# Optimization experiments

Measured on AMD Instinct MI355X. Metric: run time of the kernel, lower is better.

The kernel has to match this reference:

```python
import jax, jax.numpy as jnp
import numpy as np

B, S, D, H, DH = 2, 4096, 768, 12, 64
L = 2                      # encoder layers (reduced-depth longformer-base)
HW = 256                   # one-sided sliding window (attention_window = 512)
C = 2 * HW                 # query chunk size
NC = S // C                # number of chunks
KW = C + 2 * HW            # key-window length per chunk
V = 50265
SEP_ID, NSEP = 2, 32       # </s> token id; SEPs per block (fixed by construction)
G = NSEP + 1               # global tokens: <s> at pos 0 + all SEPs
NCLS = 5
EPS = 1e-5
NEG = -1e9


def layer_norm(x, gb):
    m = jnp.mean(x, -1, keepdims=True)
    v = jnp.var(x, -1, keepdims=True)
    return (x - m) * jax.lax.rsqrt(v + EPS) * gb[0] + gb[1]


def split_heads(x):  # [B,S,D] -> [B,H,S,DH]
    return x.reshape(B, S, H, DH).transpose(0, 2, 1, 3)


def window_gather(x):  # [B,H,S,DH] -> [B,H,NC,KW,DH] overlapping key windows
    xp = jnp.pad(x, ((0, 0), (0, 0), (HW, HW), (0, 0)))
    idx = (jnp.arange(NC) * C)[:, None] + jnp.arange(KW)[None, :]
    return xp[:, :, idx, :]


def longformer_attn(x, amask, gpos, wqkv, bqkv, wqkv_g, bqkv_g, wo, bo):
    q = split_heads(x @ wqkv[0] + bqkv[0]) / np.float32(np.sqrt(DH))
    k = split_heads(x @ wqkv[1] + bqkv[1])
    v = split_heads(x @ wqkv[2] + bqkv[2])

    # ----- local sliding-window scores (banded, chunked) -----
    kw = window_gather(k)
    vw = window_gather(v)
    qc = q.reshape(B, H, NC, C, DH)
    s_loc = jnp.einsum('bhncd,bhnkd->bhnck', qc, kw)  # [B,H,NC,C,KW]

    rel = jnp.arange(KW)[None, :] - jnp.arange(C)[:, None]          # [C,KW]
    band_ok = (rel >= 0) & (rel <= 2 * HW)
    key_pos = (jnp.arange(NC) * C)[:, None] + jnp.arange(KW)[None, :] - HW
    in_b = (key_pos >= 0) & (key_pos < S)                            # [NC,KW]
    amp = jnp.pad(amask, ((0, 0), (HW, HW)))
    idx = (jnp.arange(NC) * C)[:, None] + jnp.arange(KW)[None, :]
    am_w = amp[:, idx] > 0                                           # [B,NC,KW]
    mask = band_ok[None, None, None] & in_b[None, None, :, None, :] & am_w[:, None, :, None, :]
    s_loc = jnp.where(mask, s_loc, NEG).reshape(B, H, S, KW)

    # ----- scores of every query against the G global keys -----
    gidx = gpos[:, None, :, None]                                    # [B,1,G,1]
    kg = jnp.take_along_axis(k, gidx, axis=2)                        # [B,H,G,DH]
    vg = jnp.take_along_axis(v, gidx, axis=2)
    s_glob = jnp.einsum('bhsd,bhgd->bhsg', q, kg)                    # [B,H,S,G]

    probs = jax.nn.softmax(jnp.concatenate([s_glob, s_loc], -1), -1)
    pg, pl = probs[..., :G], probs[..., G:]
    ctx = jnp.einsum('bhsg,bhgd->bhsd', pg, vg)
    ctx = ctx + jnp.einsum('bhnck,bhnkd->bhncd', pl.reshape(B, H, NC, C, KW), vw).reshape(B, H, S, DH)

    # ----- global tokens attend to everything (separate projections) -----
    qg = split_heads(x @ wqkv_g[0] + bqkv_g[0]) / np.float32(np.sqrt(DH))
    kgf = split_heads(x @ wqkv_g[1] + bqkv_g[1])
    vgf = split_heads(x @ wqkv_g[2] + bqkv_g[2])
    qg = jnp.take_along_axis(qg, gidx, axis=2)                       # [B,H,G,DH]
    s_g = jnp.einsum('bhgd,bhsd->bhgs', qg, kgf)                     # [B,H,G,S]
    s_g = jnp.where(amask[:, None, None, :] > 0, s_g, NEG)
    og = jnp.einsum('bhgs,bhsd->bhgd', jax.nn.softmax(s_g, -1), vgf)

    ctx_m = ctx.transpose(0, 2, 1, 3).reshape(B, S, D)
    og_m = og.transpose(0, 2, 1, 3).reshape(B, G, D)
    ctx_m = ctx_m.at[jnp.arange(B)[:, None], gpos].set(og_m)         # replace global rows
    return ctx_m @ wo + bo


def setup_inputs() -> dict:
    key = jax.random.key(0)
    ks = jax.random.split(key, 12)
    ids = jax.random.randint(ks[0], (B, S), 5, V, dtype=jnp.int32)
    sep_positions = (jnp.arange(NSEP) + 1) * (S // NSEP) - 1         # SEP every 128 toks
    ids = ids.at[:, sep_positions].set(SEP_ID).at[:, 0].set(0)       # <s> at pos 0
    att = jnp.ones((B, S), jnp.int32)

    def nrm(k, shp):
        return jax.random.normal(k, shp, jnp.float32) * 0.02

    ln = jnp.stack([jnp.ones(D, jnp.float32), jnp.zeros(D, jnp.float32)])
    return dict(
        input_ids=ids, attention_mask=att,
        word_emb=nrm(ks[1], (V, D)), pos_emb=nrm(ks[2], (S + 2, D)),
        type_emb=nrm(ks[3], (D,)), emb_ln=ln,
        Wqkv=nrm(ks[4], (L, 3, D, D)), bqkv=jnp.zeros((L, 3, D), jnp.float32),
        Wqkv_g=nrm(ks[5], (L, 3, D, D)), bqkv_g=jnp.zeros((L, 3, D), jnp.float32),
        Wo=nrm(ks[6], (L, D, D)), bo=jnp.zeros((L, D), jnp.float32),
        ln1=jnp.broadcast_to(ln, (L, 2, D)),
        Wff1=nrm(ks[7], (L, D, 4 * D)), bff1=jnp.zeros((L, 4 * D), jnp.float32),
        Wff2=nrm(ks[8], (L, 4 * D, D)), bff2=jnp.zeros((L, D), jnp.float32),
        ln2=jnp.broadcast_to(ln, (L, 2, D)),
        cls_W=nrm(ks[9], (NCLS, D)), cls_b=jnp.zeros((NCLS,), jnp.float32),
    )


def reference(input_ids, attention_mask, word_emb, pos_emb, type_emb, emb_ln,
              Wqkv, bqkv, Wqkv_g, bqkv_g, Wo, bo, ln1, Wff1, bff1, Wff2, bff2,
              ln2, cls_W, cls_b):
    # global attention mask: pos 0 + every SEP (fixed count by construction)
    sep_pos = jnp.sort(jnp.where(input_ids == SEP_ID, jnp.arange(S)[None, :], S), -1)[:, :NSEP]
    sep_pos = sep_pos.astype(jnp.int32)
    gpos = jnp.concatenate([jnp.zeros((B, 1), jnp.int32), sep_pos], 1)  # [B,G]

    x = word_emb[input_ids] + pos_emb[jnp.arange(S) + 2][None] + type_emb
    x = layer_norm(x, emb_ln)
    for l in range(L):
        a = longformer_attn(x, attention_mask, gpos, Wqkv[l], bqkv[l],
                            Wqkv_g[l], bqkv_g[l], Wo[l], bo[l])
        x = layer_norm(x + a, ln1[l])
        f = jax.nn.gelu(x @ Wff1[l] + bff1[l], approximate=False) @ Wff2[l] + bff2[l]
        x = layer_norm(x + f, ln2[l])

    # gather SEP embeddings (row-major over batch then sentence) -> classifier
    h = jnp.take_along_axis(x, sep_pos[:, :, None], axis=1).reshape(B * NSEP, D)
    return h @ cls_W.T + cls_b
```

## Files before the change

kernel.cpp:

```cpp
#include <hip/hip_runtime.h>


#define Bb 2
#define Ss 4096
#define Dd 768
#define Hh 12
#define Gg 33
#define NSEPn 32
#define Ll 2
#define SPAD 4640
#define PADL 256
#define NCLSn 5
#define NCH 16
#define PARTF 1056
#define PSTR 72

typedef unsigned short u16;
typedef __attribute__((ext_vector_type(8))) short bv8;
typedef __attribute__((ext_vector_type(4))) short sv4;
typedef __attribute__((ext_vector_type(4))) float f32x4;

__device__ __forceinline__ float bf2f(u16 u) {
  unsigned v = ((unsigned)u) << 16;
  return __builtin_bit_cast(float, v);
}
__device__ __forceinline__ u16 f2bf(float f) {
  unsigned u = __builtin_bit_cast(unsigned, f);
  u += 0x7fffu + ((u >> 16) & 1u);
  return (u16)(u >> 16);
}
__device__ __forceinline__ void glds16(const void* g, void* l) {
  __builtin_amdgcn_global_load_lds(
      (const __attribute__((address_space(1))) void*)g,
      (__attribute__((address_space(3))) void*)l, 16, 0, 0);
}

__global__ void sep_find_kernel(const int* __restrict__ ids, int* __restrict__ cnt,
                                int* __restrict__ list) {
  int i = blockIdx.x * 256 + threadIdx.x;
  if (i >= Bb * Ss) return;
  int b = i >> 12;
  if (ids[i] == 2) {
    int idx = atomicAdd(&cnt[b], 1);
    if (idx < 64) list[b * 64 + idx] = i & (Ss - 1);
  }
}

__global__ void sep_sort_kernel(const int* __restrict__ cnt, const int* __restrict__ list,
                                int* __restrict__ gpos) {
  int b = blockIdx.x;
  int t = threadIdx.x;
  int n = cnt[b]; if (n > 64) n = 64;
  if (t < Gg) gpos[b * Gg + t] = (t == 0) ? 0 : (Ss - 1);
  __syncthreads();
  if (t < n) {
    int v = list[b * 64 + t];
    int rank = 0;
    for (int j = 0; j < n; ++j) rank += (list[b * 64 + j] < v) ? 1 : 0;
    if (rank < NSEPn) gpos[b * Gg + 1 + rank] = v;
  }
}

__global__ __launch_bounds__(256)
void wconv_kernel(const float* __restrict__ src0, u16* __restrict__ dst0,
                  int K, int N, int grp, int sstr, long unit, long WLs) {
  __shared__ float t[32][33];
  int z = blockIdx.z;
  const float* src = src0 + (size_t)((z / grp) * sstr + (z % grp)) * K * N;
  u16* dst = dst0 + (size_t)(z / grp) * WLs + (size_t)(z % grp) * unit;
  int n0 = blockIdx.x * 32, k0 = blockIdx.y * 32;
  int tx = threadIdx.x & 31, ty = threadIdx.x >> 5;
  #pragma unroll
  for (int i = 0; i < 4; ++i)
    t[ty + i * 8][tx] = src[(size_t)(k0 + ty + i * 8) * N + n0 + tx];
  __syncthreads();
  #pragma unroll
  for (int i = 0; i < 4; ++i)
    dst[(size_t)(n0 + ty + i * 8) * K + k0 + tx] = f2bf(t[tx][ty + i * 8]);
}

__global__ __launch_bounds__(256)
void embed_ln_kernel(const int* __restrict__ ids, const float* __restrict__ we,
                     const float* __restrict__ pe, const float* __restrict__ te,
                     const float* __restrict__ lnp, float* __restrict__ x,
                     u16* __restrict__ xb) {
  int row = blockIdx.x;
  int s = row & (Ss - 1);
  int id = ids[row];
  int tid = threadIdx.x;
  float v[3]; float sm = 0.f, s2 = 0.f;
  #pragma unroll
  for (int i = 0; i < 3; ++i) {
    int c = tid + i * 256;
    float t = we[(size_t)id * Dd + c] + pe[(size_t)(s + 2) * Dd + c] + te[c];
    v[i] = t; sm += t; s2 += t * t;
  }
  __shared__ float r1[256], r2[256];
  r1[tid] = sm; r2[tid] = s2; __syncthreads();
  for (int o = 128; o; o >>= 1) {
    if (tid < o) { r1[tid] += r1[tid + o]; r2[tid] += r2[tid + o]; }
    __syncthreads();
  }
  float mean = r1[0] * (1.f / 768.f);
  float var  = r2[0] * (1.f / 768.f) - mean * mean;
  float rs = rsqrtf(var + 1e-5f);
  #pragma unroll
  for (int i = 0; i < 3; ++i) {
    int c = tid + i * 256;
    float o = (v[i] - mean) * rs * lnp[c] + lnp[Dd + c];
    x[(size_t)row * Dd + c] = o;
    xb[(size_t)row * Dd + c] = f2bf(o);
  }
}

__global__ __launch_bounds__(256)
void add_ln3_kernel(const float* __restrict__ xin, const float* __restrict__ y0,
                    const float* __restrict__ y1, const float* __restrict__ lnp,
                    float* __restrict__ xout, u16* __restrict__ xbout) {
  int row = blockIdx.x;
  int tid = threadIdx.x;
  float v[3]; float sm = 0.f, s2 = 0.f;
  #pragma unroll
  for (int i = 0; i < 3; ++i) {
    int c = tid + i * 256;
    size_t idx = (size_t)row * Dd + c;
    float t = xin[idx] + y0[idx] + y1[idx];
    v[i] = t; sm += t; s2 += t * t;
  }
  __shared__ float r1[256], r2[256];
  r1[tid] = sm; r2[tid] = s2; __syncthreads();
  for (int o = 128; o; o >>= 1) {
    if (tid < o) { r1[tid] += r1[tid + o]; r2[tid] += r2[tid + o]; }
    __syncthreads();
  }
  float mean = r1[0] * (1.f / 768.f);
  float var  = r2[0] * (1.f / 768.f) - mean * mean;
  float rs = rsqrtf(var + 1e-5f);
  #pragma unroll
  for (int i = 0; i < 3; ++i) {
    int c = tid + i * 256;
    float o = (v[i] - mean) * rs * lnp[c] + lnp[Dd + c];
    xout[(size_t)row * Dd + c] = o;
    xbout[(size_t)row * Dd + c] = f2bf(o);
  }
}

template <int MODE>
__global__ __launch_bounds__(256)
void gemm2_kernel(const u16* __restrict__ A, const u16* __restrict__ Bt,
                  const float* __restrict__ bias, float* __restrict__ outf,
                  float* __restrict__ outf2,
                  u16* __restrict__ o0, u16* __restrict__ o1, u16* __restrict__ o2,
                  u16* __restrict__ o3, u16* __restrict__ o4,
                  int N, int Ks, int Kl, float scale) {
  __shared__ u16 la[2][128 * 32], lb[2][128 * 32];
  int tid = threadIdx.x;
  int wave = tid >> 6, lane = tid & 63;
  int wr = wave >> 1, wc = wave & 1;
  int lg = lane >> 4, lc = lane & 15;
  int row0 = blockIdx.y * 128, col0 = blockIdx.x * 128;
  int koff = blockIdx.z * Kl;

  const u16* Ag = A + (size_t)(row0 + wave * 32 + (lane >> 2)) * Ks + (lane & 3) * 8 + koff;
  const u16* Bg = Bt + (size_t)(col0 + wave * 32 + (lane >> 2)) * Ks + (lane & 3) * 8 + koff;
  int wofs = wave * 1024;

  f32x4 acc[4][4];
  #pragma unroll
  for (int m = 0; m < 4; ++m)
    #pragma unroll
    for (int n = 0; n < 4; ++n) acc[m][n] = (f32x4){0.f, 0.f, 0.f, 0.f};

  glds16(Ag, la[0] + wofs);
  glds16(Ag + (size_t)16 * Ks, la[0] + wofs + 512);
  glds16(Bg, lb[0] + wofs);
  glds16(Bg + (size_t)16 * Ks, lb[0] + wofs + 512);
  __syncthreads();

  int nk = Kl >> 5;
  for (int t = 0; t < nk; ++t) {
    int cur = t & 1;
    if (t + 1 < nk) {
      int k1 = (t + 1) << 5;
      glds16(Ag + k1, la[cur ^ 1] + wofs);
      glds16(Ag + (size_t)16 * Ks + k1, la[cur ^ 1] + wofs + 512);
      glds16(Bg + k1, lb[cur ^ 1] + wofs);
      glds16(Bg + (size_t)16 * Ks + k1, lb[cur ^ 1] + wofs + 512);
    }
    bv8 af[4], bf_[4];
    #pragma unroll
    for (int m = 0; m < 4; ++m)
      af[m] = *reinterpret_cast<const bv8*>(la[cur] + (wr * 64 + m * 16 + lc) * 32 + lg * 8);
    #pragma unroll
    for (int n = 0; n < 4; ++n)
      bf_[n] = *reinterpret_cast<const bv8*>(lb[cur] + (wc * 64 + n * 16 + lc) * 32 + lg * 8);
    __builtin_amdgcn_s_setprio(1);
    #pragma unroll
    for (int m = 0; m < 4; ++m)
      #pragma unroll
      for (int n = 0; n < 4; ++n)
        acc[m][n] = __builtin_amdgcn_mfma_f32_16x16x32_bf16(af[m], bf_[n], acc[m][n], 0, 0, 0);
    __builtin_amdgcn_s_setprio(0);
    __syncthreads();
  }

  #pragma unroll
  for (int m = 0; m < 4; ++m) {
    int grow0 = row0 + wr * 64 + m * 16 + lg * 4;
    #pragma unroll
    for (int n = 0; n < 4; ++n) {
      int gcol = col0 + wc * 64 + n * 16 + lc;
      float bvl = bias[gcol];
      if (MODE == 0) {
        float* od = blockIdx.z ? outf2 : outf;
        float badd = blockIdx.z ? 0.f : bvl;
        #pragma unroll
        for (int r = 0; r < 4; ++r)
          od[(size_t)(grow0 + r) * N + gcol] = acc[m][n][r] + badd;
      } else if (MODE == 1) {
        #pragma unroll
        for (int r = 0; r < 4; ++r) {
          float v = acc[m][n][r] + bvl;
          v = 0.5f * v * (1.0f + erff(v * 0.70710678118654752f));
          o0[(size_t)(grow0 + r) * N + gcol] = f2bf(v);
        }
      } else if (MODE == 4) {
        #pragma unroll
        for (int r = 0; r < 4; ++r)
          o0[(size_t)(grow0 + r) * N + gcol] = f2bf((acc[m][n][r] + bvl) * scale);
      } else if (MODE == 2) {
        int sec = (col0 >> 7) / 6;
        int colr = gcol - sec * 768;
        int hh = colr >> 6, d = colr & 63;
        int bb = grow0 >> 12, s = grow0 & (Ss - 1);
        size_t bhh = (size_t)(bb * Hh + hh);
        if (sec == 0) {
          #pragma unroll
          for (int r = 0; r < 4; ++r)
            o0[(bhh * Ss + s + r) * 64 + d] = f2bf((acc[m][n][r] + bvl) * scale);
        } else if (sec == 1) {
          #pragma unroll
          for (int r = 0; r < 4; ++r)
            o1[(bhh * SPAD + PADL + s + r) * 64 + d] = f2bf(acc[m][n][r] + bvl);
        } else if (sec == 2) {
          sv4 pk;
          #pragma unroll
          for (int r = 0; r < 4; ++r) pk[r] = (short)f2bf(acc[m][n][r] + bvl);
          *reinterpret_cast<sv4*>(o2 + (bhh * 64 + d) * SPAD + PADL + s) = pk;
        } else if (sec == 3) {
          #pragma unroll
          for (int r = 0; r < 4; ++r)
            o3[(bhh * Ss + s + r) * 64 + d] = f2bf(acc[m][n][r] + bvl);
        } else {
          sv4 pk;
          #pragma unroll
          for (int r = 0; r < 4; ++r) pk[r] = (short)f2bf(acc[m][n][r] + bvl);
          *reinterpret_cast<sv4*>(o4 + (bhh * 64 + d) * Ss + s) = pk;
        }
      }
    }
  }
}

__global__ __launch_bounds__(256)
void gather_glob_kernel(const u16* __restrict__ kpk, const u16* __restrict__ vtpk,
                        const int* __restrict__ gpos, u16* __restrict__ kg,
                        u16* __restrict__ vgt) {
  int bh = blockIdx.x;
  int b = bh / Hh;
  int tid = threadIdx.x;
  for (int idx = tid; idx < 64 * 64; idx += 256) {
    int g = idx >> 6, d = idx & 63;
    u16 kv = 0, vv = 0;
    if (g < Gg) {
      int p = gpos[b * Gg + g];
      kv = kpk[((size_t)bh * SPAD + PADL + p) * 64 + d];
      vv = vtpk[((size_t)bh * 64 + d) * SPAD + PADL + p];
    }
    kg[(size_t)bh * 4096 + idx] = kv;
    vgt[((size_t)bh * 64 + d) * 64 + g] = vv;
  }
}

__global__ __launch_bounds__(256)
void gather_xg_kernel(const u16* __restrict__ xb, const int* __restrict__ gpos,
                      u16* __restrict__ xg) {
  int rg = blockIdx.x;
  int b = rg / Gg;
  int p = gpos[rg];
  int tid = threadIdx.x;
  for (int c = tid; c < Dd; c += 256)
    xg[(size_t)rg * Dd + c] = xb[((size_t)b * Ss + p) * Dd + c];
}

#define LOCAL_NB (Bb * Hh * (Ss / 64))
__global__ __launch_bounds__(256)
void attn_local_kernel(const u16* __restrict__ qpk, const u16* __restrict__ kpk,
                       const u16* __restrict__ vtpk, const u16* __restrict__ kg,
                       const u16* __restrict__ vgt, const int* __restrict__ amask,
                       u16* __restrict__ ctx) {
  __shared__ u16 Plds[4][16 * PSTR];
  int bid = blockIdx.x;
  int swz = (bid & 7) * (LOCAL_NB / 8) + (bid >> 3);
  int qb = swz & 63;
  int bh = swz >> 6;
  int b = bh / Hh;
  int h = bh - b * Hh;
  int wv = threadIdx.x >> 6;
  int q0 = qb * 64 + wv * 16;
  int lane = threadIdx.x & 63;
  int lg = lane >> 4, lc = lane & 15;
  int lg4 = lg * 4;
  int q = q0 + lc;

  const u16* qbase = qpk + (((size_t)bh) * Ss + q0) * 64;
  bv8 aq0 = *reinterpret_cast<const bv8*>(qbase + (size_t)lc * 64 + lg * 8);
  bv8 aq1 = *reinterpret_cast<const bv8*>(qbase + (size_t)lc * 64 + 32 + lg * 8);

  f32x4 o[4];
  #pragma unroll
  for (int i = 0; i < 4; ++i) o[i] = (f32x4){0.f, 0.f, 0.f, 0.f};
  float mrun = -1e30f, lrun = 0.f;

  const u16* kgb = kg + ((size_t)bh) * 64 * 64;
  const u16* vgb = vgt + ((size_t)bh) * 64 * 64;
  const u16* kb = kpk + ((size_t)bh) * SPAD * 64;
  const u16* vb = vtpk + ((size_t)bh) * 64 * SPAD;
  const int* amb = amask + b * Ss;
  u16* P = &Plds[wv][0];

  bv8 kc[8];
  #pragma unroll
  for (int j = 0; j < 4; ++j) {
    const u16* kr = kgb + (size_t)(j * 16 + lc) * 64;
    kc[2 * j]     = *reinterpret_cast<const bv8*>(kr + lg * 8);
    kc[2 * j + 1] = *reinterpret_cast<const bv8*>(kr + 32 + lg * 8);
  }
  int amvN;
  { int ni = min(max(q0 - 256 + lane, 0), Ss - 1); amvN = amb[ni]; }

  for (int step = 0; step < 10; ++step) {
    bool isg = (step == 0);
    int ks = isg ? 0 : (q0 - 256 + (step - 1) * 64);
    int amvC = amvN;
    if (step < 9) { int ni = min(max(q0 - 256 + step * 64 + lane, 0), Ss - 1); amvN = amb[ni]; }

    bv8 vf[8];
    #pragma unroll
    for (int j2 = 0; j2 < 2; ++j2)
      #pragma unroll
      for (int nt = 0; nt < 4; ++nt) {
        const u16* vr = isg ? (vgb + (size_t)(nt * 16 + lc) * 64 + j2 * 32)
                            : (vb + (size_t)(nt * 16 + lc) * SPAD + PADL + ks + j2 * 32);
        vf[j2 * 4 + nt] = *reinterpret_cast<const bv8*>(vr + lg * 8);
      }
    unsigned long long kmask;
    if (isg) {
      kmask = (1ull << Gg) - 1;
    } else {
      int kidx = ks + lane;
      kmask = __ballot((kidx >= 0) && (kidx < Ss) && (amvC > 0));
    }
    f32x4 sc[4];
    __builtin_amdgcn_s_setprio(1);
    #pragma unroll
    for (int j = 0; j < 4; ++j) {
      f32x4 z = (f32x4){0.f, 0.f, 0.f, 0.f};
      sc[j] = __builtin_amdgcn_mfma_f32_16x16x32_bf16(kc[2 * j], aq0, z, 0, 0, 0);
      sc[j] = __builtin_amdgcn_mfma_f32_16x16x32_bf16(kc[2 * j + 1], aq1, sc[j], 0, 0, 0);
    }
    __builtin_amdgcn_s_setprio(0);
    if (step < 9) {
      int ksn = q0 - 256 + step * 64;
      #pragma unroll
      for (int j = 0; j < 4; ++j) {
        const u16* kr = kb + (size_t)(PADL + ksn + j * 16 + lc) * 64;
        kc[2 * j]     = *reinterpret_cast<const bv8*>(kr + lg * 8);
        kc[2 * j + 1] = *reinterpret_cast<const bv8*>(kr + 32 + lg * 8);
      }
    }
    float mloc = -1e30f;
    bool fast = (!isg) && (step >= 2) && (step <= 8) && (kmask == ~0ull);
    if (fast) {
      #pragma unroll
      for (int j = 0; j < 4; ++j)
        #pragma unroll
        for (int r = 0; r < 4; ++r) mloc = fmaxf(mloc, sc[j][r]);
    } else {
      #pragma unroll
      for (int j = 0; j < 4; ++j)
        #pragma unroll
        for (int r = 0; r < 4; ++r) {
          int kk = ks + j * 16 + lg4 + r;
          bool ok = (kmask >> (j * 16 + lg4 + r)) & 1;
          if (!isg) ok = ok && ((unsigned)(kk - q + 256) <= 512u);
          sc[j][r] = ok ? sc[j][r] : -1e9f;
          mloc = fmaxf(mloc, sc[j][r]);
        }
    }
    mloc = fmaxf(mloc, __shfl_xor(mloc, 16));
    mloc = fmaxf(mloc, __shfl_xor(mloc, 32));
    if (__any(mloc > mrun)) {
      float nm = fmaxf(mrun, mloc);
      float scal = __expf(mrun - nm);
      mrun = nm;
      lrun *= scal;
      #pragma unroll
      for (int r = 0; r < 4; ++r) {
        float sr = __shfl(scal, lg4 + r);
        #pragma unroll
        for (int nt = 0; nt < 4; ++nt) o[nt][r] *= sr;
      }
    }
    float psum = 0.f;
    #pragma unroll
    for (int j = 0; j < 4; ++j) {
      sv4 pk;
      #pragma unroll
      for (int r = 0; r < 4; ++r) {
        float p = __expf(sc[j][r] - mrun);
        psum += p;
        pk[r] = (short)f2bf(p);
      }
      *reinterpret_cast<sv4*>(P + lc * PSTR + j * 16 + lg4) = pk;
    }
    psum += __shfl_xor(psum, 16);
    psum += __shfl_xor(psum, 32);
    lrun += psum;
    __builtin_amdgcn_s_setprio(1);
    #pragma unroll
    for (int j2 = 0; j2 < 2; ++j2) {
      bv8 ap = *reinterpret_cast<const bv8*>(P + lc * PSTR + j2 * 32 + lg * 8);
      #pragma unroll
      for (int nt = 0; nt < 4; ++nt)
        o[nt] = __builtin_amdgcn_mfma_f32_16x16x32_bf16(ap, vf[j2 * 4 + nt], o[nt], 0, 0, 0);
    }
    __builtin_amdgcn_s_setprio(0);
  }
  float inv = 1.0f / lrun;
  #pragma unroll
  for (int r = 0; r < 4; ++r) {
    float invr = __shfl(inv, lg4 + r);
    size_t rowoff = ((size_t)b * Ss + q0 + lg4 + r) * Dd + h * 64;
    #pragma unroll
    for (int nt = 0; nt < 4; ++nt)
      ctx[rowoff + nt * 16 + lc] = f2bf(o[nt][r] * invr);
  }
}

__global__ __launch_bounds__(192)
void attn_globalq_kernel(const u16* __restrict__ qgb, const u16* __restrict__ kgf,
                         const u16* __restrict__ vgt, const int* __restrict__ amask,
                         float* __restrict__ part) {
  __shared__ u16 Plds[3][16 * 32];
  int blk = blockIdx.x;
  int ch = blk & (NCH - 1);
  int bh = blk / NCH;
  int b = bh / Hh, h = bh - b * Hh;
  int wv = threadIdx.x >> 6;
  int lane = threadIdx.x & 63;
  int lg = lane >> 4, lc = lane & 15;

  int qrow = wv * 16 + lc;
  bv8 aq0 = (bv8)0, aq1 = (bv8)0;
  if (qrow < Gg) {
    const u16* qr = qgb + (size_t)(b * Gg + qrow) * Dd + h * 64;
    aq0 = *reinterpret_cast<const bv8*>(qr + lg * 8);
    aq1 = *reinterpret_cast<const bv8*>(qr + 32 + lg * 8);
  }

  f32x4 o[4];
  float mrun[4], lrun[4];
  #pragma unroll
  for (int i = 0; i < 4; ++i) { o[i] = (f32x4){0.f,0.f,0.f,0.f}; mrun[i] = -1e30f; lrun[i] = 0.f; }

  const u16* kb = kgf + ((size_t)bh) * Ss * 64;
  const u16* vb = vgt + ((size_t)bh) * 64 * Ss;
  const int* amb = amask + b * Ss;
  int ks0 = ch * (Ss / NCH);

  for (int st = 0; st < (Ss / NCH) / 32; ++st) {
    int ks = ks0 + st * 32;
    f32x4 sc0, sc1;
    {
      const u16* kr0 = kb + (size_t)(ks + lc) * 64;
      const u16* kr1 = kr0 + 16 * 64;
      bv8 b00 = *reinterpret_cast<const bv8*>(kr0 + lg * 8);
      bv8 b01 = *reinterpret_cast<const bv8*>(kr0 + 32 + lg * 8);
      bv8 b10 = *reinterpret_cast<const bv8*>(kr1 + lg * 8);
      bv8 b11 = *reinterpret_cast<const bv8*>(kr1 + 32 + lg * 8);
      f32x4 z = (f32x4){0.f,0.f,0.f,0.f};
      sc0 = __builtin_amdgcn_mfma_f32_16x16x32_bf16(aq0, b00, z, 0, 0, 0);
      sc0 = __builtin_amdgcn_mfma_f32_16x16x32_bf16(aq1, b01, sc0, 0, 0, 0);
      sc1 = __builtin_amdgcn_mfma_f32_16x16x32_bf16(aq0, b10, z, 0, 0, 0);
      sc1 = __builtin_amdgcn_mfma_f32_16x16x32_bf16(aq1, b11, sc1, 0, 0, 0);
    }
    bool v0 = amb[ks + lc] > 0;
    bool v1 = amb[ks + 16 + lc] > 0;
    #pragma unroll
    for (int r = 0; r < 4; ++r) {
      float s0 = v0 ? sc0[r] : -1e9f;
      float s1 = v1 ? sc1[r] : -1e9f;
      float rm = fmaxf(s0, s1);
      #pragma unroll
      for (int off = 1; off < 16; off <<= 1) rm = fmaxf(rm, __shfl_xor(rm, off));
      float nm = fmaxf(mrun[r], rm);
      float scal = __expf(mrun[r] - nm);
      float p0 = __expf(s0 - nm);
      float p1 = __expf(s1 - nm);
      float ps = p0 + p1;
      #pragma unroll
      for (int off = 1; off < 16; off <<= 1) ps += __shfl_xor(ps, off);
      lrun[r] = lrun[r] * scal + ps;
      mrun[r] = nm;
      #pragma unroll
      for (int nt = 0; nt < 4; ++nt) o[nt][r] *= scal;
      int prow = lg * 4 + r;
      Plds[wv][prow * 32 + lc] = f2bf(p0);
      Plds[wv][prow * 32 + 16 + lc] = f2bf(p1);
    }
    bv8 ap = *reinterpret_cast<const bv8*>(&Plds[wv][lc * 32 + lg * 8]);
    #pragma unroll
    for (int nt = 0; nt < 4; ++nt) {
      const u16* vr = vb + (size_t)(nt * 16 + lc) * Ss + ks;
      bv8 bvv = *reinterpret_cast<const bv8*>(vr + lg * 8);
      o[nt] = __builtin_amdgcn_mfma_f32_16x16x32_bf16(ap, bvv, o[nt], 0, 0, 0);
    }
  }

  float* pb = part + ((size_t)(bh * 3 + wv) * NCH + ch) * PARTF;
  #pragma unroll
  for (int r = 0; r < 4; ++r) {
    int row = lg * 4 + r;
    #pragma unroll
    for (int nt = 0; nt < 4; ++nt)
      pb[row * 64 + nt * 16 + lc] = o[nt][r];
    if (lc == 0) {
      pb[1024 + row] = mrun[r];
      pb[1040 + row] = lrun[r];
    }
  }
}

__global__ __launch_bounds__(256)
void attn_gmerge_kernel(const float* __restrict__ part, const int* __restrict__ gpos,
                        u16* __restrict__ ctx) {
  __shared__ float wgt[Gg][NCH];
  __shared__ float sinvl[Gg];
  int bh = blockIdx.x;
  int b = bh / Hh, h = bh - b * Hh;
  int tid = threadIdx.x;
  if (tid < Gg) {
    int qt = tid >> 4, rr = tid & 15;
    const float* pb = part + ((size_t)(bh * 3 + qt) * NCH) * PARTF;
    float mx = -1e30f;
    for (int c = 0; c < NCH; ++c) mx = fmaxf(mx, pb[c * PARTF + 1024 + rr]);
    float l = 0.f;
    for (int c = 0; c < NCH; ++c) {
      float w = __expf(pb[c * PARTF + 1024 + rr] - mx);
      wgt[tid][c] = w;
      l += w * pb[c * PARTF + 1040 + rr];
    }
    sinvl[tid] = 1.0f / l;
  }
  __syncthreads();
  for (int e = tid; e < Gg * 64; e += 256) {
    int row = e >> 6, d = e & 63;
    int qt = row >> 4, rr = row & 15;
    const float* pb = part + ((size_t)(bh * 3 + qt) * NCH) * PARTF + rr * 64 + d;
    float acc = 0.f;
    #pragma unroll
    for (int c = 0; c < NCH; ++c) acc += wgt[row][c] * pb[c * PARTF];
    int pos = gpos[b * Gg + row];
    ctx[((size_t)b * Ss + pos) * Dd + h * 64 + d] = f2bf(acc * sinvl[row]);
  }
}

__global__ __launch_bounds__(64)
void cls_kernel(const float* __restrict__ x, const float* __restrict__ W,
                const float* __restrict__ bias, const int* __restrict__ gpos,
                float* __restrict__ out) {
  int r = blockIdx.x;
  int b = r >> 5, i = r & 31;
  int pos = gpos[b * Gg + 1 + i];
  int lane = threadIdx.x;
  const float* xr = x + ((size_t)b * Ss + pos) * Dd;
  float acc[NCLSn] = {0.f, 0.f, 0.f, 0.f, 0.f};
  for (int k = lane; k < Dd; k += 64) {
    float xv = xr[k];
    #pragma unroll
    for (int c = 0; c < NCLSn; ++c) acc[c] += xv * W[c * Dd + k];
  }
  #pragma unroll
  for (int c = 0; c < NCLSn; ++c) {
    #pragma unroll
    for (int off = 1; off < 64; off <<= 1) acc[c] += __shfl_xor(acc[c], off);
  }
  if (lane == 0) {
    #pragma unroll
    for (int c = 0; c < NCLSn; ++c) out[r * NCLSn + c] = acc[c] + bias[c];
  }
}

extern "C" void kernel_launch(void* const* d_in, const int* in_sizes, int n_in,
                              void* d_out, int out_size, void* d_ws, size_t ws_size,
                              hipStream_t stream) {
  const int* ids     = (const int*)d_in[0];
  const int* amask   = (const int*)d_in[1];
  const float* we    = (const float*)d_in[2];
  const float* pe    = (const float*)d_in[3];
  const float* te    = (const float*)d_in[4];
  const float* embln = (const float*)d_in[5];
  const float* Wqkv  = (const float*)d_in[6];
  const float* bqkv  = (const float*)d_in[7];
  const float* Wqkvg = (const float*)d_in[8];
  const float* bqkvg = (const float*)d_in[9];
  const float* Wo    = (const float*)d_in[10];
  const float* bo    = (const float*)d_in[11];
  const float* ln1   = (const float*)d_in[12];
  const float* Wff1  = (const float*)d_in[13];
  const float* bff1  = (const float*)d_in[14];
  const float* Wff2  = (const float*)d_in[15];
  const float* bff2  = (const float*)d_in[16];
  const float* ln2   = (const float*)d_in[17];
  const float* clsW  = (const float*)d_in[18];
  const float* clsb  = (const float*)d_in[19];
  float* out = (float*)d_out;

  char* ws = (char*)d_ws;
  size_t off = 0;
  auto alloc = [&](size_t bytes) { size_t o = off; off += (bytes + 255) & ~(size_t)255; return o; };

  const size_t DD = (size_t)Dd * Dd;
  const size_t DF = (size_t)Dd * 4 * Dd;
  const size_t WL = 7 * DD + 2 * DF;

  size_t o_cnt  = alloc(Bb * 4);
  size_t o_list = alloc(Bb * 64 * 4);
  size_t o_gpos = alloc(Bb * Gg * 4);
  size_t o_bias = alloc((size_t)Ll * 3840 * 4);
  size_t o_w    = alloc(WL * Ll * 2);
  size_t o_x    = alloc((size_t)Bb * Ss * Dd * 4);
  size_t o_xb   = alloc((size_t)Bb * Ss * Dd * 2);
  size_t o_kgf  = alloc((size_t)Bb * Hh * Ss * 64 * 2);
  size_t o_vgf  = alloc((size_t)Bb * Hh * Ss * 64 * 2);
  size_t o_accB = o_kgf;
  size_t o_qpk  = alloc((size_t)Bb * Hh * Ss * 64 * 2);
  size_t o_kpk  = alloc((size_t)Bb * Hh * SPAD * 64 * 2);
  size_t o_vtpk = alloc((size_t)Bb * Hh * 64 * SPAD * 2);
  size_t o_kg   = alloc((size_t)Bb * Hh * 64 * 64 * 2);
  size_t o_vgt  = alloc((size_t)Bb * Hh * 64 * 64 * 2);
  size_t o_xg   = alloc((size_t)128 * Dd * 2);
  size_t o_qg   = alloc((size_t)128 * Dd * 2);
  size_t o_part = alloc((size_t)Bb * Hh * 3 * NCH * PARTF * 4);
  size_t o_f1b  = o_qpk;
  {
    size_t f1b_bytes = (size_t)Bb * Ss * 4 * Dd * 2;
    if (off - o_qpk < f1b_bytes) off = o_qpk + ((f1b_bytes + 255) & ~(size_t)255);
  }
  size_t o_ctx = alloc((size_t)Bb * Ss * Dd * 2);
  size_t o_acc = alloc((size_t)Bb * Ss * Dd * 4);
  if (ws_size < off) return;

  u16* Wb = (u16*)(ws + o_w);
  int* gposp = (int*)(ws + o_gpos);
  float* accA = (float*)(ws + o_acc);
  float* accB = (float*)(ws + o_accB);

  (void)hipMemsetAsync(ws + o_cnt, 0, Bb * 4, stream);
  (void)hipMemsetAsync(ws + o_kpk, 0, (size_t)Bb * Hh * SPAD * 64 * 2, stream);
  (void)hipMemsetAsync(ws + o_vtpk, 0, (size_t)Bb * Hh * 64 * SPAD * 2, stream);
  (void)hipMemsetAsync(ws + o_xg, 0, (size_t)128 * Dd * 2, stream);

  for (int l = 0; l < Ll; ++l) {
    (void)hipMemcpyAsync(ws + o_bias + (size_t)l * 3840 * 4, bqkv + (size_t)l * 3 * Dd,
                         3 * Dd * 4, hipMemcpyDeviceToDevice, stream);
    (void)hipMemcpyAsync(ws + o_bias + (size_t)l * 3840 * 4 + 3 * Dd * 4,
                         bqkvg + (size_t)(l * 3 + 1) * Dd,
                         2 * Dd * 4, hipMemcpyDeviceToDevice, stream);
  }

  sep_find_kernel<<<(Bb * Ss + 255) / 256, 256, 0, stream>>>(ids, (int*)(ws + o_cnt), (int*)(ws + o_list));
  sep_sort_kernel<<<Bb, 64, 0, stream>>>((int*)(ws + o_cnt), (int*)(ws + o_list), gposp);

  wconv_kernel<<<dim3(24, 24, 6), 256, 0, stream>>>(Wqkv,       Wb,          Dd, Dd, 3, 3, (long)DD, (long)WL);
  wconv_kernel<<<dim3(24, 24, 2), 256, 0, stream>>>(Wqkvg + DD,     Wb + 3 * DD, Dd, Dd, 1, 3, 0L, (long)WL);
  wconv_kernel<<<dim3(24, 24, 2), 256, 0, stream>>>(Wqkvg + 2 * DD, Wb + 4 * DD, Dd, Dd, 1, 3, 0L, (long)WL);
  wconv_kernel<<<dim3(24, 24, 2), 256, 0, stream>>>(Wqkvg,          Wb + 5 * DD, Dd, Dd, 1, 3, 0L, (long)WL);
  wconv_kernel<<<dim3(24, 24, 2), 256, 0, stream>>>(Wo,         Wb + 6 * DD, Dd, Dd, 1, 1, 0L, (long)WL);
  wconv_kernel<<<dim3(96, 24, 2), 256, 0, stream>>>(Wff1,       Wb + 7 * DD, Dd, 4 * Dd, 1, 1, 0L, (long)WL);
  wconv_kernel<<<dim3(24, 96, 2), 256, 0, stream>>>(Wff2,       Wb + 7 * DD + DF, 4 * Dd, Dd, 1, 1, 0L, (long)WL);

  embed_ln_kernel<<<Bb * Ss, 256, 0, stream>>>(ids, we, pe, te, embln, (float*)(ws + o_x), (u16*)(ws + o_xb));

  for (int l = 0; l < Ll; ++l) {
    size_t wb = (size_t)l * WL;
    u16* xb = (u16*)(ws + o_xb);
    gemm2_kernel<2><<<dim3(30, 64), 256, 0, stream>>>(xb, Wb + wb, (float*)(ws + o_bias) + (size_t)l * 3840,
        nullptr, nullptr,
        (u16*)(ws + o_qpk), (u16*)(ws + o_kpk), (u16*)(ws + o_vtpk),
        (u16*)(ws + o_kgf), (u16*)(ws + o_vgf), 3840, Dd, Dd, 0.125f);
    gather_glob_kernel<<<Bb * Hh, 256, 0, stream>>>((u16*)(ws + o_kpk), (u16*)(ws + o_vtpk), gposp, (u16*)(ws + o_kg), (u16*)(ws + o_vgt));
    gather_xg_kernel<<<Bb * Gg, 256, 0, stream>>>(xb, gposp, (u16*)(ws + o_xg));
    gemm2_kernel<4><<<dim3(6, 1), 256, 0, stream>>>((u16*)(ws + o_xg), Wb + wb + 5 * DD, bqkvg + (size_t)l * 3 * Dd,
        nullptr, nullptr, (u16*)(ws + o_qg), nullptr, nullptr, nullptr, nullptr, Dd, Dd, Dd, 0.125f);
    attn_local_kernel<<<LOCAL_NB, 256, 0, stream>>>((u16*)(ws + o_qpk), (u16*)(ws + o_kpk), (u16*)(ws + o_vtpk), (u16*)(ws + o_kg), (u16*)(ws + o_vgt), amask, (u16*)(ws + o_ctx));
    attn_globalq_kernel<<<Bb * Hh * NCH, 192, 0, stream>>>((u16*)(ws + o_qg), (u16*)(ws + o_kgf), (u16*)(ws + o_vgf), amask, (float*)(ws + o_part));
    attn_gmerge_kernel<<<Bb * Hh, 256, 0, stream>>>((float*)(ws + o_part), gposp, (u16*)(ws + o_ctx));
    gemm2_kernel<0><<<dim3(6, 64, 2), 256, 0, stream>>>((u16*)(ws + o_ctx), Wb + wb + 6 * DD, bo + (size_t)l * Dd, accA, accB,
        nullptr, nullptr, nullptr, nullptr, nullptr, Dd, Dd, Dd / 2, 1.0f);
    add_ln3_kernel<<<Bb * Ss, 256, 0, stream>>>((float*)(ws + o_x), accA, accB, ln1 + (size_t)l * 2 * Dd, (float*)(ws + o_x), xb);
    gemm2_kernel<1><<<dim3(24, 64), 256, 0, stream>>>(xb, Wb + wb + 7 * DD, bff1 + (size_t)l * 4 * Dd, nullptr, nullptr,
        (u16*)(ws + o_f1b), nullptr, nullptr, nullptr, nullptr, 4 * Dd, Dd, Dd, 1.0f);
    gemm2_kernel<0><<<dim3(6, 64, 2), 256, 0, stream>>>((u16*)(ws + o_f1b), Wb + wb + 7 * DD + DF, bff2 + (size_t)l * Dd, accA, accB,
        nullptr, nullptr, nullptr, nullptr, nullptr, Dd, 4 * Dd, 2 * Dd, 1.0f);
    add_ln3_kernel<<<Bb * Ss, 256, 0, stream>>>((float*)(ws + o_x), accA, accB, ln2 + (size_t)l * 2 * Dd, (float*)(ws + o_x), xb);
  }

  cls_kernel<<<Bb * NSEPn, 64, 0, stream>>>((float*)(ws + o_x), clsW, clsb, gposp, out);
}
```

Baseline: 875.7 us.

## Triple-buffer GEMM LDS tiles with prefetch distance two and partial vmcnt waits

Moves the bf16 GEMM main loop from double to triple LDS buffering, issuing global-to-LDS loads two K-steps ahead. The full syncthreads is replaced by an explicit s_waitcnt vmcnt(4) plus s_barrier, so only the oldest tile's loads must land before each step. This is meant to hide more global memory latency behind the MFMA work. It raises LDS use from 32KB to 48KB per block, which can lower occupancy, and it relies on hand-counted vmcnt values that are correct only if the compiler issues no other vector memory ops in the loop.

```diff
diff --git a/kernel.cpp b/kernel.cpp
--- a/kernel.cpp
+++ b/kernel.cpp
@@ -153,7 +153,7 @@
                   u16* __restrict__ o0, u16* __restrict__ o1, u16* __restrict__ o2,
                   u16* __restrict__ o3, u16* __restrict__ o4,
                   int N, int Ks, int Kl, float scale) {
-  __shared__ u16 la[2][128 * 32], lb[2][128 * 32];
+  __shared__ u16 la[3][128 * 32], lb[3][128 * 32];
   int tid = threadIdx.x;
   int wave = tid >> 6, lane = tid & 63;
   int wr = wave >> 1, wc = wave & 1;
@@ -171,21 +171,33 @@
     #pragma unroll
     for (int n = 0; n < 4; ++n) acc[m][n] = (f32x4){0.f, 0.f, 0.f, 0.f};
 
-  glds16(Ag, la[0] + wofs);
-  glds16(Ag + (size_t)16 * Ks, la[0] + wofs + 512);
-  glds16(Bg, lb[0] + wofs);
-  glds16(Bg + (size_t)16 * Ks, lb[0] + wofs + 512);
-  __syncthreads();
-
   int nk = Kl >> 5;
+  {
+    glds16(Ag, la[0] + wofs);
+    glds16(Ag + (size_t)16 * Ks, la[0] + wofs + 512);
+    glds16(Bg, lb[0] + wofs);
+    glds16(Bg + (size_t)16 * Ks, lb[0] + wofs + 512);
+    if (nk > 1) {
+      glds16(Ag + 32, la[1] + wofs);
+      glds16(Ag + (size_t)16 * Ks + 32, la[1] + wofs + 512);
+      glds16(Bg + 32, lb[1] + wofs);
+      glds16(Bg + (size_t)16 * Ks + 32, lb[1] + wofs + 512);
+      asm volatile("s_waitcnt vmcnt(4)" ::: "memory");
+    } else {
+      asm volatile("s_waitcnt vmcnt(0)" ::: "memory");
+    }
+    __builtin_amdgcn_s_barrier();
+  }
+
   for (int t = 0; t < nk; ++t) {
-    int cur = t & 1;
-    if (t + 1 < nk) {
-      int k1 = (t + 1) << 5;
-      glds16(Ag + k1, la[cur ^ 1] + wofs);
-      glds16(Ag + (size_t)16 * Ks + k1, la[cur ^ 1] + wofs + 512);
-      glds16(Bg + k1, lb[cur ^ 1] + wofs);
-      glds16(Bg + (size_t)16 * Ks + k1, lb[cur ^ 1] + wofs + 512);
+    int cur = t % 3;
+    if (t + 2 < nk) {
+      int k2 = (t + 2) << 5;
+      int nb = (t + 2) % 3;
+      glds16(Ag + k2, la[nb] + wofs);
+      glds16(Ag + (size_t)16 * Ks + k2, la[nb] + wofs + 512);
+      glds16(Bg + k2, lb[nb] + wofs);
+      glds16(Bg + (size_t)16 * Ks + k2, lb[nb] + wofs + 512);
     }
     bv8 af[4], bf_[4];
     #pragma unroll
@@ -201,7 +213,11 @@
       for (int n = 0; n < 4; ++n)
         acc[m][n] = __builtin_amdgcn_mfma_f32_16x16x32_bf16(af[m], bf_[n], acc[m][n], 0, 0, 0);
     __builtin_amdgcn_s_setprio(0);
-    __syncthreads();
+    if (t + 1 < nk) {
+      if (t + 2 < nk) asm volatile("s_waitcnt vmcnt(4)" ::: "memory");
+      else            asm volatile("s_waitcnt vmcnt(0)" ::: "memory");
+      __builtin_amdgcn_s_barrier();
+    }
   }
 
   #pragma unroll
```

Result: no change. 887.8 us (+1.4%).

## Add 256x256-tile GEMM for QKV and FFN1, swizzle LDS layout

Applied to the files above, without the earlier changes.

Adds a 512-thread GEMM kernel with 256x256 output tiles (8x4 MFMA fragments per wave) and routes the large QKV projection and FFN1 GEMMs to it. This raises arithmetic intensity per LDS load and cuts global reloads of A and B. Both GEMM kernels also XOR-swizzle the 16-byte chunk placement in LDS to reduce bank conflicts on fragment reads. The QKV grid drops to 480 blocks and FFN1 to 384 blocks, which may leave the 256 CUs unevenly loaded. The larger accumulator set also raises register pressure.

```diff
diff --git a/kernel.cpp b/kernel.cpp
--- a/kernel.cpp
+++ b/kernel.cpp
@@ -149,9 +149,7 @@
 __global__ __launch_bounds__(256)
 void gemm2_kernel(const u16* __restrict__ A, const u16* __restrict__ Bt,
                   const float* __restrict__ bias, float* __restrict__ outf,
-                  float* __restrict__ outf2,
-                  u16* __restrict__ o0, u16* __restrict__ o1, u16* __restrict__ o2,
-                  u16* __restrict__ o3, u16* __restrict__ o4,
+                  float* __restrict__ outf2, u16* __restrict__ o0,
                   int N, int Ks, int Kl, float scale) {
   __shared__ u16 la[2][128 * 32], lb[2][128 * 32];
   int tid = threadIdx.x;
@@ -161,9 +159,11 @@
   int row0 = blockIdx.y * 128, col0 = blockIdx.x * 128;
   int koff = blockIdx.z * Kl;
 
-  const u16* Ag = A + (size_t)(row0 + wave * 32 + (lane >> 2)) * Ks + (lane & 3) * 8 + koff;
-  const u16* Bg = Bt + (size_t)(col0 + wave * 32 + (lane >> 2)) * Ks + (lane & 3) * 8 + koff;
+  int sgr = (lane & 3) ^ ((lane >> 3) & 3);
+  const u16* Ag = A + (size_t)(row0 + wave * 32 + (lane >> 2)) * Ks + sgr * 8 + koff;
+  const u16* Bg = Bt + (size_t)(col0 + wave * 32 + (lane >> 2)) * Ks + sgr * 8 + koff;
   int wofs = wave * 1024;
+  int gph = (lg ^ ((lc >> 1) & 3)) * 8;
 
   f32x4 acc[4][4];
   #pragma unroll
@@ -190,10 +190,10 @@
     bv8 af[4], bf_[4];
     #pragma unroll
     for (int m = 0; m < 4; ++m)
-      af[m] = *reinterpret_cast<const bv8*>(la[cur] + (wr * 64 + m * 16 + lc) * 32 + lg * 8);
+      af[m] = *reinterpret_cast<const bv8*>(la[cur] + (wr * 64 + m * 16 + lc) * 32 + gph);
     #pragma unroll
     for (int n = 0; n < 4; ++n)
-      bf_[n] = *reinterpret_cast<const bv8*>(lb[cur] + (wc * 64 + n * 16 + lc) * 32 + lg * 8);
+      bf_[n] = *reinterpret_cast<const bv8*>(lb[cur] + (wc * 64 + n * 16 + lc) * 32 + gph);
     __builtin_amdgcn_s_setprio(1);
     #pragma unroll
     for (int m = 0; m < 4; ++m)
@@ -217,19 +217,98 @@
         #pragma unroll
         for (int r = 0; r < 4; ++r)
           od[(size_t)(grow0 + r) * N + gcol] = acc[m][n][r] + badd;
-      } else if (MODE == 1) {
+      } else {
+        #pragma unroll
+        for (int r = 0; r < 4; ++r)
+          o0[(size_t)(grow0 + r) * N + gcol] = f2bf((acc[m][n][r] + bvl) * scale);
+      }
+    }
+  }
+}
+
+template <int MODE>
+__global__ __launch_bounds__(512, 2)
+void gemm3_kernel(const u16* __restrict__ A, const u16* __restrict__ Bt,
+                  const float* __restrict__ bias,
+                  u16* __restrict__ o0, u16* __restrict__ o1, u16* __restrict__ o2,
+                  u16* __restrict__ o3, u16* __restrict__ o4,
+                  int N, int K, float scale) {
+  __shared__ u16 SA[2][8192], SB[2][8192];
+  int tid = threadIdx.x;
+  int w = tid >> 6, lane = tid & 63;
+  int wm = w >> 2, wn = w & 3;
+  int lg = lane >> 4, lc = lane & 15;
+  int row0 = blockIdx.y * 256, col0 = blockIdx.x * 256;
+
+  int srow = tid >> 2;
+  int sgr  = (tid & 3) ^ ((tid >> 3) & 3);
+  const u16* Ag0 = A + (size_t)(row0 + srow) * K + sgr * 8;
+  const u16* Ag1 = Ag0 + (size_t)128 * K;
+  const u16* Bg0 = Bt + (size_t)(col0 + srow) * K + sgr * 8;
+  const u16* Bg1 = Bg0 + (size_t)128 * K;
+  int wofs = w * 512;
+  int gph = (lg ^ ((lc >> 1) & 3)) * 8;
+
+  f32x4 acc[8][4];
+  #pragma unroll
+  for (int m = 0; m < 8; ++m)
+    #pragma unroll
+    for (int n = 0; n < 4; ++n) acc[m][n] = (f32x4){0.f, 0.f, 0.f, 0.f};
+
+  glds16(Ag0, &SA[0][wofs]);
+  glds16(Ag1, &SA[0][4096 + wofs]);
+  glds16(Bg0, &SB[0][wofs]);
+  glds16(Bg1, &SB[0][4096 + wofs]);
+  __syncthreads();
+
+  const int nk = K >> 5;
+  const u16* pa_base;
+  const u16* pb_base;
+  int brow = (wn & 1) * 64;
+  for (int t = 0; t < nk; ++t) {
+    int cur = t & 1;
+    if (t + 1 < nk) {
+      int k1 = (t + 1) << 5;
+      glds16(Ag0 + k1, &SA[cur ^ 1][wofs]);
+      glds16(Ag1 + k1, &SA[cur ^ 1][4096 + wofs]);
+      glds16(Bg0 + k1, &SB[cur ^ 1][wofs]);
+      glds16(Bg1 + k1, &SB[cur ^ 1][4096 + wofs]);
+    }
+    pa_base = &SA[cur][wm * 4096];
+    pb_base = &SB[cur][(wn >> 1) * 4096];
+    bv8 af[8], bf_[4];
+    #pragma unroll
+    for (int fm = 0; fm < 8; ++fm)
+      af[fm] = *reinterpret_cast<const bv8*>(pa_base + (fm * 16 + lc) * 32 + gph);
+    #pragma unroll
+    for (int fn = 0; fn < 4; ++fn)
+      bf_[fn] = *reinterpret_cast<const bv8*>(pb_base + (brow + fn * 16 + lc) * 32 + gph);
+    __builtin_amdgcn_s_setprio(1);
+    #pragma unroll
+    for (int fm = 0; fm < 8; ++fm)
+      #pragma unroll
+      for (int fn = 0; fn < 4; ++fn)
+        acc[fm][fn] = __builtin_amdgcn_mfma_f32_16x16x32_bf16(af[fm], bf_[fn], acc[fm][fn], 0, 0, 0);
+    __builtin_amdgcn_s_setprio(0);
+    __syncthreads();
+  }
+
+  int sec = (MODE == 2) ? (col0 / 768) : 0;
+  #pragma unroll
+  for (int fm = 0; fm < 8; ++fm) {
+    int grow0 = row0 + wm * 128 + fm * 16 + lg * 4;
+    #pragma unroll
+    for (int fn = 0; fn < 4; ++fn) {
+      int gcol = col0 + wn * 64 + fn * 16 + lc;
+      float bvl = bias[gcol];
+      if (MODE == 1) {
         #pragma unroll
         for (int r = 0; r < 4; ++r) {
-          float v = acc[m][n][r] + bvl;
+          float v = acc[fm][fn][r] + bvl;
           v = 0.5f * v * (1.0f + erff(v * 0.70710678118654752f));
           o0[(size_t)(grow0 + r) * N + gcol] = f2bf(v);
         }
-      } else if (MODE == 4) {
-        #pragma unroll
-        for (int r = 0; r < 4; ++r)
-          o0[(size_t)(grow0 + r) * N + gcol] = f2bf((acc[m][n][r] + bvl) * scale);
-      } else if (MODE == 2) {
-        int sec = (col0 >> 7) / 6;
+      } else {
         int colr = gcol - sec * 768;
         int hh = colr >> 6, d = colr & 63;
         int bb = grow0 >> 12, s = grow0 & (Ss - 1);
@@ -237,24 +316,24 @@
         if (sec == 0) {
           #pragma unroll
           for (int r = 0; r < 4; ++r)
-            o0[(bhh * Ss + s + r) * 64 + d] = f2bf((acc[m][n][r] + bvl) * scale);
+            o0[(bhh * Ss + s + r) * 64 + d] = f2bf((acc[fm][fn][r] + bvl) * scale);
         } else if (sec == 1) {
           #pragma unroll
           for (int r = 0; r < 4; ++r)
-            o1[(bhh * SPAD + PADL + s + r) * 64 + d] = f2bf(acc[m][n][r] + bvl);
+            o1[(bhh * SPAD + PADL + s + r) * 64 + d] = f2bf(acc[fm][fn][r] + bvl);
         } else if (sec == 2) {
           sv4 pk;
           #pragma unroll
-          for (int r = 0; r < 4; ++r) pk[r] = (short)f2bf(acc[m][n][r] + bvl);
+          for (int r = 0; r < 4; ++r) pk[r] = (short)f2bf(acc[fm][fn][r] + bvl);
           *reinterpret_cast<sv4*>(o2 + (bhh * 64 + d) * SPAD + PADL + s) = pk;
         } else if (sec == 3) {
           #pragma unroll
           for (int r = 0; r < 4; ++r)
-            o3[(bhh * Ss + s + r) * 64 + d] = f2bf(acc[m][n][r] + bvl);
+            o3[(bhh * Ss + s + r) * 64 + d] = f2bf(acc[fm][fn][r] + bvl);
         } else {
           sv4 pk;
           #pragma unroll
-          for (int r = 0; r < 4; ++r) pk[r] = (short)f2bf(acc[m][n][r] + bvl);
+          for (int r = 0; r < 4; ++r) pk[r] = (short)f2bf(acc[fm][fn][r] + bvl);
           *reinterpret_cast<sv4*>(o4 + (bhh * 64 + d) * Ss + s) = pk;
         }
       }
@@ -696,24 +775,23 @@
   for (int l = 0; l < Ll; ++l) {
     size_t wb = (size_t)l * WL;
     u16* xb = (u16*)(ws + o_xb);
-    gemm2_kernel<2><<<dim3(30, 64), 256, 0, stream>>>(xb, Wb + wb, (float*)(ws + o_bias) + (size_t)l * 3840,
-        nullptr, nullptr,
+    gemm3_kernel<2><<<dim3(15, 32), 512, 0, stream>>>(xb, Wb + wb, (float*)(ws + o_bias) + (size_t)l * 3840,
         (u16*)(ws + o_qpk), (u16*)(ws + o_kpk), (u16*)(ws + o_vtpk),
-        (u16*)(ws + o_kgf), (u16*)(ws + o_vgf), 3840, Dd, Dd, 0.125f);
+        (u16*)(ws + o_kgf), (u16*)(ws + o_vgf), 3840, Dd, 0.125f);
     gather_glob_kernel<<<Bb * Hh, 256, 0, stream>>>((u16*)(ws + o_kpk), (u16*)(ws + o_vtpk), gposp, (u16*)(ws + o_kg), (u16*)(ws + o_vgt));
     gather_xg_kernel<<<Bb * Gg, 256, 0, stream>>>(xb, gposp, (u16*)(ws + o_xg));
     gemm2_kernel<4><<<dim3(6, 1), 256, 0, stream>>>((u16*)(ws + o_xg), Wb + wb + 5 * DD, bqkvg + (size_t)l * 3 * Dd,
-        nullptr, nullptr, (u16*)(ws + o_qg), nullptr, nullptr, nullptr, nullptr, Dd, Dd, Dd, 0.125f);
+        nullptr, nullptr, (u16*)(ws + o_qg), Dd, Dd, Dd, 0.125f);
     attn_local_kernel<<<LOCAL_NB, 256, 0, stream>>>((u16*)(ws + o_qpk), (u16*)(ws + o_kpk), (u16*)(ws + o_vtpk), (u16*)(ws + o_kg), (u16*)(ws + o_vgt), amask, (u16*)(ws + o_ctx));
     attn_globalq_kernel<<<Bb * Hh * NCH, 192, 0, stream>>>((u16*)(ws + o_qg), (u16*)(ws + o_kgf), (u16*)(ws + o_vgf), amask, (float*)(ws + o_part));
     attn_gmerge_kernel<<<Bb * Hh, 256, 0, stream>>>((float*)(ws + o_part), gposp, (u16*)(ws + o_ctx));
     gemm2_kernel<0><<<dim3(6, 64, 2), 256, 0, stream>>>((u16*)(ws + o_ctx), Wb + wb + 6 * DD, bo + (size_t)l * Dd, accA, accB,
-        nullptr, nullptr, nullptr, nullptr, nullptr, Dd, Dd, Dd / 2, 1.0f);
+        nullptr, Dd, Dd, Dd / 2, 1.0f);
     add_ln3_kernel<<<Bb * Ss, 256, 0, stream>>>((float*)(ws + o_x), accA, accB, ln1 + (size_t)l * 2 * Dd, (float*)(ws + o_x), xb);
-    gemm2_kernel<1><<<dim3(24, 64), 256, 0, stream>>>(xb, Wb + wb + 7 * DD, bff1 + (size_t)l * 4 * Dd, nullptr, nullptr,
-        (u16*)(ws + o_f1b), nullptr, nullptr, nullptr, nullptr, 4 * Dd, Dd, Dd, 1.0f);
+    gemm3_kernel<1><<<dim3(12, 32), 512, 0, stream>>>(xb, Wb + wb + 7 * DD, bff1 + (size_t)l * 4 * Dd,
+        (u16*)(ws + o_f1b), nullptr, nullptr, nullptr, nullptr, 4 * Dd, Dd, 1.0f);
     gemm2_kernel<0><<<dim3(6, 64, 2), 256, 0, stream>>>((u16*)(ws + o_f1b), Wb + wb + 7 * DD + DF, bff2 + (size_t)l * Dd, accA, accB,
-        nullptr, nullptr, nullptr, nullptr, nullptr, Dd, 4 * Dd, 2 * Dd, 1.0f);
+        nullptr, Dd, 4 * Dd, 2 * Dd, 1.0f);
     add_ln3_kernel<<<Bb * Ss, 256, 0, stream>>>((float*)(ws + o_x), accA, accB, ln2 + (size_t)l * 2 * Dd, (float*)(ws + o_x), xb);
   }
 
```

Measured after the change: 932.7 us. +6.5%, slower.
